# Kernel optimization log

Measured on AMD Instinct MI355X. Metric: run time of the kernel, lower is better.

Reference implementation:

```python
import jax, jax.numpy as jnp
import numpy as np

WINDOW_SIZE = 11
SIGMA = 1.5
C1 = 0.01 ** 2
C2 = 0.03 ** 2


def _gaussian_window(window_size, sigma, channel, dtype=jnp.float32):
    x = np.arange(window_size) - window_size // 2
    g = np.exp(-(x.astype(np.float64) ** 2) / (2.0 * sigma ** 2))
    g = (g / g.sum()).astype(np.float32)
    w2d = np.outer(g, g)  # [K, K]
    # depthwise kernel: [C, 1, K, K] (OIHW with feature_group_count=C)
    w = np.broadcast_to(w2d, (channel, 1, window_size, window_size))
    return jnp.asarray(w, dtype=dtype)


def _dw_conv(x, window):
    # x: [B, C, H, W]; window: [C, 1, K, K]; SAME padding via pad=K//2 (K odd)
    k = window.shape[-1]
    p = k // 2
    return jax.lax.conv_general_dilated(
        x, window,
        window_strides=(1, 1),
        padding=((p, p), (p, p)),
        dimension_numbers=("NCHW", "OIHW", "NCHW"),
        feature_group_count=x.shape[1],
    )


def setup_inputs() -> dict:
    key = jax.random.key(0)
    k1, k2 = jax.random.split(key)
    shape = (32, 3, 512, 512)
    img1 = jax.random.uniform(k1, shape, dtype=jnp.float32)
    img2 = jax.random.uniform(k2, shape, dtype=jnp.float32)
    return {"img1": img1, "img2": img2}


def reference(img1, img2):
    channel = img1.shape[1]
    window = _gaussian_window(WINDOW_SIZE, SIGMA, channel, img1.dtype)

    mu1 = _dw_conv(img1, window)
    mu2 = _dw_conv(img2, window)
    mu1_sq = mu1 * mu1
    mu2_sq = mu2 * mu2
    mu1_mu2 = mu1 * mu2

    sigma1_sq = _dw_conv(img1 * img1, window) - mu1_sq
    sigma2_sq = _dw_conv(img2 * img2, window) - mu2_sq
    sigma12 = _dw_conv(img1 * img2, window) - mu1_mu2

    ssim_map = ((2.0 * mu1_mu2 + C1) * (2.0 * sigma12 + C2)) / (
        (mu1_sq + mu2_sq + C1) * (sigma1_sq + sigma2_sq + C2)
    )
    return 1.0 - jnp.mean(ssim_map)
```

## Files before the change

### kernel.cpp

```cpp
#include <hip/hip_runtime.h>

#define HH 512
#define WW 512
#define PLANES 96
#define RSTRIP 32
#define NPIX 25165824.0f

#define G0 0.2660117f
#define G1 0.2130056f
#define G2 0.1093607f
#define G3 0.0360008f
#define G4 0.0075988f
#define G5 0.0010284f

#define C1F 1e-4f
#define C2F 9e-4f

#define DECL_HIST(Z) float Z##0=0.f,Z##1=0.f,Z##2=0.f,Z##3=0.f,Z##4=0.f,Z##5=0.f,\
                           Z##6=0.f,Z##7=0.f,Z##8=0.f,Z##9=0.f,Z##10=0.f
#define SHIFT_HIST(Z) do{Z##0=Z##1;Z##1=Z##2;Z##2=Z##3;Z##3=Z##4;Z##4=Z##5;\
                         Z##5=Z##6;Z##6=Z##7;Z##7=Z##8;Z##8=Z##9;Z##9=Z##10;}while(0)
#define VCONV(Z) fmaf(G5, Z##0+Z##10, fmaf(G4, Z##1+Z##9, fmaf(G3, Z##2+Z##8,\
                 fmaf(G2, Z##3+Z##7, fmaf(G1, Z##4+Z##6, G0*Z##5)))))

__global__ __launch_bounds__(256) __attribute__((amdgpu_waves_per_eu(7, 8)))
void ssim_main(const float* __restrict__ img1,
               const float* __restrict__ img2,
               float* __restrict__ acc) {
    __shared__ float lx[2][272], ly[2][272];
    const int tid = threadIdx.x;
    const int c0  = blockIdx.x * 256;
    const int r0  = blockIdx.y * RSTRIP;
    const int p   = blockIdx.z;
    const size_t pb = (size_t)p * (HH * WW);

    const int cs = c0 - 5 + tid;
    const bool in_main = (unsigned)cs < (unsigned)WW;
    const bool halo    = tid < 10;
    const bool in_halo = halo && (unsigned)(cs + 256) < (unsigned)WW;

    const float* rx = img1 + pb + (ptrdiff_t)(r0 - 5) * WW + cs;
    const float* ry = img2 + pb + (ptrdiff_t)(r0 - 5) * WW + cs;

    DECL_HIST(A); DECL_HIST(B); DECL_HIST(P); DECL_HIST(Q);

    float lsum = 0.f;

#pragma unroll 2
    for (int t = r0 - 5; t <= r0 + RSTRIP + 4; ++t, rx += WW, ry += WW) {
        SHIFT_HIST(A); SHIFT_HIST(B); SHIFT_HIST(P); SHIFT_HIST(Q);

        float nA = 0.f, nB = 0.f, nP = 0.f, nQ = 0.f;
        if ((unsigned)t < (unsigned)HH) {
            const int buf = t & 1;
            float sx = 0.f, sy = 0.f, hx = 0.f, hy = 0.f;
            if (in_main) { sx = rx[0];   sy = ry[0];   }
            if (in_halo) { hx = rx[256]; hy = ry[256]; }
            lx[buf][tid] = sx;  ly[buf][tid] = sy;
            if (halo) { lx[buf][tid + 256] = hx; ly[buf][tid + 256] = hy; }
            __syncthreads();

            const float* bx = &lx[buf][tid];
            const float* by = &ly[buf][tid];
            {
                const float x5 = bx[5], y5 = by[5];
                const float u = x5 + y5, v = x5 - y5;
                nA = G0 * u;       nB = G0 * v;
                nP = G0 * (u * u); nQ = G0 * (v * v);
            }
#define HPAIR(KL, KR, GK) { \
            const float xl = bx[KL], yl = by[KL], xr = bx[KR], yr = by[KR]; \
            const float ul = xl + yl, vl = xl - yl, ur = xr + yr, vr = xr - yr; \
            nA = fmaf(GK, ul + ur, nA); nP = fmaf(GK, fmaf(ul, ul, ur * ur), nP); \
            nB = fmaf(GK, vl + vr, nB); nQ = fmaf(GK, fmaf(vl, vl, vr * vr), nQ); }
            HPAIR(4, 6, G1) HPAIR(3, 7, G2) HPAIR(2, 8, G3)
            HPAIR(1, 9, G4) HPAIR(0, 10, G5)
#undef HPAIR
        }
        A10 = nA; B10 = nB; P10 = nP; Q10 = nQ;

        const int s = t - 5 - r0;
        if ((unsigned)s < (unsigned)RSTRIP) {
            const float mu_u = VCONV(A);
            const float mu_v = VCONV(B);
            const float cu2  = VCONV(P);
            const float cv2  = VCONV(Q);
            const float a = mu_u * mu_u;
            const float b = mu_v * mu_v;
            const float musq = 0.5f  * (a + b);
            const float mu12 = 0.25f * (a - b);
            const float csq  = 0.5f  * (cu2 + cv2);
            const float cxy  = 0.25f * (cu2 - cv2);
            const float ssum = csq - musq;
            const float s12  = cxy - mu12;
            const float num = fmaf(2.f, mu12, C1F) * fmaf(2.f, s12, C2F);
            const float den = (musq + C1F) * (ssum + C2F);
            lsum += num * __builtin_amdgcn_rcpf(den);
        }
    }

#pragma unroll
    for (int off = 32; off > 0; off >>= 1)
        lsum += __shfl_down(lsum, off, 64);
    __shared__ float ws4[4];
    const int lane = threadIdx.x & 63;
    const int wv   = threadIdx.x >> 6;
    if (lane == 0) ws4[wv] = lsum;
    __syncthreads();
    if (threadIdx.x == 0)
        atomicAdd(acc, ws4[0] + ws4[1] + ws4[2] + ws4[3]);
}

__global__ void ssim_zero(float* acc) { acc[0] = 0.f; }

__global__ void ssim_finalize(const float* __restrict__ acc, float* __restrict__ out) {
    out[0] = 1.f - acc[0] * (1.f / NPIX);
}

extern "C" void kernel_launch(void* const* d_in, const int* in_sizes, int n_in,
                              void* d_out, int out_size, void* d_ws, size_t ws_size,
                              hipStream_t stream) {
    const float* img1 = (const float*)d_in[0];
    const float* img2 = (const float*)d_in[1];
    float* out = (float*)d_out;
    float* acc = (float*)d_ws;

    ssim_zero<<<1, 1, 0, stream>>>(acc);
    dim3 grid(WW / 256, HH / RSTRIP, PLANES);
    ssim_main<<<grid, 256, 0, stream>>>(img1, img2, acc);
    ssim_finalize<<<1, 1, 0, stream>>>(acc, out);
}
```

Measured before the change: 279.3 us.

## Precompute u/v into interleaved LDS and use packed float2 FMA math

Each thread now computes u=x+y and v=x−y once while staging data, and stores them as interleaved float2 in a single LDS array. Neighbours previously recomputed them for every tap. The horizontal and vertical convolutions run on 2-wide vectors so the compiler can emit packed FP32 instructions (v_pk_fma_f32), and each LDS read becomes a 64-bit load. The occupancy hint is relaxed from 7 to 6 waves per EU to give the packed register pairs more room. The risk is lower occupancy and possible LDS bank conflicts with 8-byte accesses.

```diff
diff --git a/kernel.cpp b/kernel.cpp
--- a/kernel.cpp
+++ b/kernel.cpp
@@ -16,18 +16,21 @@
 #define C1F 1e-4f
 #define C2F 9e-4f
 
-#define DECL_HIST(Z) float Z##0=0.f,Z##1=0.f,Z##2=0.f,Z##3=0.f,Z##4=0.f,Z##5=0.f,\
-                           Z##6=0.f,Z##7=0.f,Z##8=0.f,Z##9=0.f,Z##10=0.f
+typedef float v2f __attribute__((ext_vector_type(2)));
+#define PKFMA(a, b, c) __builtin_elementwise_fma(a, b, c)
+
+#define DECL_HIST2(Z) v2f Z##0={0,0},Z##1={0,0},Z##2={0,0},Z##3={0,0},Z##4={0,0},\
+                          Z##5={0,0},Z##6={0,0},Z##7={0,0},Z##8={0,0},Z##9={0,0},Z##10={0,0}
 #define SHIFT_HIST(Z) do{Z##0=Z##1;Z##1=Z##2;Z##2=Z##3;Z##3=Z##4;Z##4=Z##5;\
                          Z##5=Z##6;Z##6=Z##7;Z##7=Z##8;Z##8=Z##9;Z##9=Z##10;}while(0)
-#define VCONV(Z) fmaf(G5, Z##0+Z##10, fmaf(G4, Z##1+Z##9, fmaf(G3, Z##2+Z##8,\
-                 fmaf(G2, Z##3+Z##7, fmaf(G1, Z##4+Z##6, G0*Z##5)))))
+#define VCONV2(Z) PKFMA(g5, Z##0+Z##10, PKFMA(g4, Z##1+Z##9, PKFMA(g3, Z##2+Z##8,\
+                  PKFMA(g2, Z##3+Z##7, PKFMA(g1, Z##4+Z##6, g0*Z##5)))))
 
-__global__ __launch_bounds__(256) __attribute__((amdgpu_waves_per_eu(7, 8)))
+__global__ __launch_bounds__(256) __attribute__((amdgpu_waves_per_eu(6, 8)))
 void ssim_main(const float* __restrict__ img1,
                const float* __restrict__ img2,
                float* __restrict__ acc) {
-    __shared__ float lx[2][272], ly[2][272];
+    __shared__ v2f luv[2][272];
     const int tid = threadIdx.x;
     const int c0  = blockIdx.x * 256;
     const int r0  = blockIdx.y * RSTRIP;
@@ -42,55 +45,53 @@
     const float* rx = img1 + pb + (ptrdiff_t)(r0 - 5) * WW + cs;
     const float* ry = img2 + pb + (ptrdiff_t)(r0 - 5) * WW + cs;
 
-    DECL_HIST(A); DECL_HIST(B); DECL_HIST(P); DECL_HIST(Q);
+    const v2f g0 = {G0, G0}, g1 = {G1, G1}, g2 = {G2, G2},
+              g3 = {G3, G3}, g4 = {G4, G4}, g5 = {G5, G5};
+
+    DECL_HIST2(AB); DECL_HIST2(PQ);
 
     float lsum = 0.f;
 
 #pragma unroll 2
     for (int t = r0 - 5; t <= r0 + RSTRIP + 4; ++t, rx += WW, ry += WW) {
-        SHIFT_HIST(A); SHIFT_HIST(B); SHIFT_HIST(P); SHIFT_HIST(Q);
+        SHIFT_HIST(AB); SHIFT_HIST(PQ);
 
-        float nA = 0.f, nB = 0.f, nP = 0.f, nQ = 0.f;
+        v2f nAB = {0.f, 0.f}, nPQ = {0.f, 0.f};
         if ((unsigned)t < (unsigned)HH) {
             const int buf = t & 1;
             float sx = 0.f, sy = 0.f, hx = 0.f, hy = 0.f;
             if (in_main) { sx = rx[0];   sy = ry[0];   }
             if (in_halo) { hx = rx[256]; hy = ry[256]; }
-            lx[buf][tid] = sx;  ly[buf][tid] = sy;
-            if (halo) { lx[buf][tid + 256] = hx; ly[buf][tid + 256] = hy; }
+            luv[buf][tid] = v2f{sx + sy, sx - sy};
+            if (halo) luv[buf][tid + 256] = v2f{hx + hy, hx - hy};
             __syncthreads();
 
-            const float* bx = &lx[buf][tid];
-            const float* by = &ly[buf][tid];
+            const v2f* w = &luv[buf][tid];
             {
-                const float x5 = bx[5], y5 = by[5];
-                const float u = x5 + y5, v = x5 - y5;
-                nA = G0 * u;       nB = G0 * v;
-                nP = G0 * (u * u); nQ = G0 * (v * v);
+                const v2f uv5 = w[5];
+                nAB = g0 * uv5;
+                nPQ = g0 * (uv5 * uv5);
             }
 #define HPAIR(KL, KR, GK) { \
-            const float xl = bx[KL], yl = by[KL], xr = bx[KR], yr = by[KR]; \
-            const float ul = xl + yl, vl = xl - yl, ur = xr + yr, vr = xr - yr; \
-            nA = fmaf(GK, ul + ur, nA); nP = fmaf(GK, fmaf(ul, ul, ur * ur), nP); \
-            nB = fmaf(GK, vl + vr, nB); nQ = fmaf(GK, fmaf(vl, vl, vr * vr), nQ); }
-            HPAIR(4, 6, G1) HPAIR(3, 7, G2) HPAIR(2, 8, G3)
-            HPAIR(1, 9, G4) HPAIR(0, 10, G5)
+            const v2f l = w[KL], r = w[KR]; \
+            nAB = PKFMA(GK, l + r, nAB); \
+            nPQ = PKFMA(GK, PKFMA(l, l, r * r), nPQ); }
+            HPAIR(4, 6, g1) HPAIR(3, 7, g2) HPAIR(2, 8, g3)
+            HPAIR(1, 9, g4) HPAIR(0, 10, g5)
 #undef HPAIR
         }
-        A10 = nA; B10 = nB; P10 = nP; Q10 = nQ;
+        AB10 = nAB; PQ10 = nPQ;
 
         const int s = t - 5 - r0;
         if ((unsigned)s < (unsigned)RSTRIP) {
-            const float mu_u = VCONV(A);
-            const float mu_v = VCONV(B);
-            const float cu2  = VCONV(P);
-            const float cv2  = VCONV(Q);
-            const float a = mu_u * mu_u;
-            const float b = mu_v * mu_v;
+            const v2f mu = VCONV2(AB);
+            const v2f c2 = VCONV2(PQ);
+            const float a = mu.x * mu.x;
+            const float b = mu.y * mu.y;
             const float musq = 0.5f  * (a + b);
             const float mu12 = 0.25f * (a - b);
-            const float csq  = 0.5f  * (cu2 + cv2);
-            const float cxy  = 0.25f * (cu2 - cv2);
+            const float csq  = 0.5f  * (c2.x + c2.y);
+            const float cxy  = 0.25f * (c2.x - c2.y);
             const float ssum = csq - musq;
             const float s12  = cxy - mu12;
             const float num = fmaf(2.f, mu12, C1F) * fmaf(2.f, s12, C2F);
```

After: 272.4 us. 2.5% less time.
